# Optimization experiments

Hardware: AMD Instinct MI355X
Metric: run time of the kernel (lower is better)

Reference implementation:

```python
import jax, jax.numpy as jnp
import numpy as np

B, V, D = 8, 2048, 3
CL1_F, CL1_K = 64, 6
CL2_F, CL2_K = 128, 5
F1, F2 = 512, 256


def _uniform(k, shape, fin, fout):
    s = np.sqrt(2.0 / (fin + fout)).astype(np.float32)
    return jax.random.uniform(k, shape, jnp.float32, -s, s)


def setup_inputs() -> dict:
    key = jax.random.key(0)
    ks = jax.random.split(key, 8)
    x = jax.random.normal(ks[0], (B, D, V), jnp.float32)
    # dense stand-in for the scaled graph Laplacian; scaled so spectral radius < 1
    L = jax.random.normal(ks[1], (B, V, V), jnp.float32) * (0.5 / np.sqrt(V))
    L = 0.5 * (L + L.transpose(0, 2, 1))  # symmetric like a real Laplacian
    return {
        "x": x,
        "L": L,
        "cl1_w": _uniform(ks[2], (CL1_F, D * CL1_K), CL1_K, CL1_F),
        "cl1_b": jnp.zeros((CL1_F,), jnp.float32),
        "cl2_w": _uniform(ks[3], (CL2_F, CL2_K * CL1_F), CL2_K * CL1_F, CL2_F),
        "cl2_b": jnp.zeros((CL2_F,), jnp.float32),
        "fc1_w": _uniform(ks[4], (F1, CL2_F), CL2_F, F1),
        "fc1_b": jnp.zeros((F1,), jnp.float32),
        "fc2_w": _uniform(ks[5], (F2, F1), F1, F2),
        "fc2_b": jnp.zeros((F2,), jnp.float32),
    }


def _cheby_conv(x, L, W, b, K):
    # x: [B, V, Fin], L: [B, V, V] -> [B, V, Fout]
    x0 = x
    xs = [x0]
    if K > 1:
        x1 = jnp.einsum('bvu,buf->bvf', L, x0)
        xs.append(x1)
    for _ in range(2, K):
        x2 = 2.0 * jnp.einsum('bvu,buf->bvf', L, x1) - x0
        xs.append(x2)
        x0, x1 = x1, x2
    # torch ordering: feature index = fin * K + k  -> stack K on last axis
    xk = jnp.stack(xs, axis=-1)                 # [B, V, Fin, K]
    xk = xk.reshape(xk.shape[0], xk.shape[1], -1)  # [B, V, Fin*K]
    return xk @ W.T + b


def reference(x, L, cl1_w, cl1_b, cl2_w, cl2_b, fc1_w, fc1_b, fc2_w, fc2_b):
    xp = x.transpose(0, 2, 1)                    # [B, V, D]
    y = jax.nn.relu(_cheby_conv(xp, L, cl1_w, cl1_b, CL1_K))
    y = jax.nn.relu(_cheby_conv(y, L, cl2_w, cl2_b, CL2_K))
    y = jax.nn.relu(y @ fc1_w.T + fc1_b)
    y = jax.nn.relu(y @ fc2_w.T + fc2_b)
    return y                                     # [B, V, F2]
```

## Files before the change

### kernel.cpp

```cpp
#include <hip/hip_runtime.h>

#define B_ 8
#define V_ 2048
#define D_ 3
#define M_ (B_*V_)

typedef __attribute__((ext_vector_type(8))) short short8;
typedef __attribute__((ext_vector_type(4))) float f32x4;

__device__ inline void async_copy16(const void* g, void* lds) {
  __builtin_amdgcn_global_load_lds(
      (const __attribute__((address_space(1))) unsigned int*)g,
      (__attribute__((address_space(3))) unsigned int*)lds, 16, 0, 0);
}

__device__ inline void split_bf16(float v, short& hi, short& lo) {
  unsigned u  = __float_as_uint(v);
  unsigned hb = u & 0xFFFF0000u;
  float d = v - __uint_as_float(hb);
  hi = (short)(hb >> 16);
  lo = (short)(__float_as_uint(d) >> 16);
}

__global__ __launch_bounds__(256) void k_prep(
    const float* __restrict__ x,
    const float* __restrict__ w1, const float* __restrict__ w2,
    const float* __restrict__ fw1, const float* __restrict__ fw2,
    float* __restrict__ xa,
    short* __restrict__ XKh, short* __restrict__ XKl,
    short* __restrict__ w1h, short* __restrict__ w1l,
    short* __restrict__ w2h, short* __restrict__ w2l,
    short* __restrict__ fw1h, short* __restrict__ fw1l,
    short* __restrict__ fw2h, short* __restrict__ fw2l) {
  int i = blockIdx.x * 256 + threadIdx.x;
  short hi, lo;
  if (i < M_*64) {
    int r = i >> 6, s = i & 63;
    float val = 0.f;
    if (s == 0 || s == 6 || s == 12) {
      int f = s / 6;
      int b = r >> 11, v = r & (V_-1);
      val = x[((size_t)b*D_ + f)*V_ + v];
      xa[(size_t)r*3 + f] = val;
    }
    split_bf16(val, hi, lo);
    XKh[i] = hi; XKl[i] = lo;
    return;
  }
  i -= M_*64;
  if (i < 4096) {
    int n = i >> 6, k = i & 63;
    float v = (k < 18) ? w1[n*18 + k] : 0.f;
    split_bf16(v, hi, lo); w1h[i] = hi; w1l[i] = lo; return;
  }
  i -= 4096;
  if (i < 40960) { split_bf16(w2[i],  hi, lo); w2h[i]=hi;  w2l[i]=lo;  return; }
  i -= 40960;
  if (i < 65536) { split_bf16(fw1[i], hi, lo); fw1h[i]=hi; fw1l[i]=lo; return; }
  i -= 65536;
  if (i < 131072){ split_bf16(fw2[i], hi, lo); fw2h[i]=hi; fw2l[i]=lo; return; }
}

__global__ __launch_bounds__(256) void k_cheby1(const float* __restrict__ L,
    const float* __restrict__ xc, const float* __restrict__ xp,
    float* __restrict__ xn, short* __restrict__ XKh, short* __restrict__ XKl,
    float alpha, float beta, int kidx) {
  __shared__ float sx[3][V_];
  int b  = blockIdx.x >> 7;
  int r0 = (blockIdx.x & 127) * 16;
  const float* xcb = xc + (size_t)b*V_*D_;
  for (int i = threadIdx.x; i < V_*D_; i += 256) {
    int u = i / 3, f = i - u*3;
    sx[f][u] = xcb[i];
  }
  __syncthreads();
  int w = threadIdx.x >> 6, lane = threadIdx.x & 63;
  const float4* X0 = (const float4*)sx[0];
  const float4* X1 = (const float4*)sx[1];
  const float4* X2 = (const float4*)sx[2];
  int rbase = r0 + w*4;
  const float4* Lr[4];
  #pragma unroll
  for (int rr = 0; rr < 4; rr++)
    Lr[rr] = (const float4*)(L + ((size_t)b*V_ + rbase + rr)*V_);

  float acc[4][3] = {{0.f,0.f,0.f},{0.f,0.f,0.f},{0.f,0.f,0.f},{0.f,0.f,0.f}};

  #pragma unroll 2
  for (int it = 0; it < 8; it++) {
    int u4 = it*64 + lane;
    float4 x0 = X0[u4], x1 = X1[u4], x2 = X2[u4];
    #pragma unroll
    for (int rr = 0; rr < 4; rr++) {
      float4 lv = Lr[rr][u4];
      acc[rr][0] = fmaf(lv.x,x0.x,fmaf(lv.y,x0.y,fmaf(lv.z,x0.z,fmaf(lv.w,x0.w,acc[rr][0]))));
      acc[rr][1] = fmaf(lv.x,x1.x,fmaf(lv.y,x1.y,fmaf(lv.z,x1.z,fmaf(lv.w,x1.w,acc[rr][1]))));
      acc[rr][2] = fmaf(lv.x,x2.x,fmaf(lv.y,x2.y,fmaf(lv.z,x2.z,fmaf(lv.w,x2.w,acc[rr][2]))));
    }
  }
  #pragma unroll
  for (int off = 32; off > 0; off >>= 1)
    #pragma unroll
    for (int rr = 0; rr < 4; rr++)
      #pragma unroll
      for (int f = 0; f < 3; f++)
        acc[rr][f] += __shfl_down(acc[rr][f], off);

  if (lane == 0) {
    size_t base = ((size_t)b*V_ + rbase)*3;
    float v[12];
    #pragma unroll
    for (int rr = 0; rr < 4; rr++)
      #pragma unroll
      for (int f = 0; f < 3; f++)
        v[rr*3+f] = alpha*acc[rr][f];
    if (beta != 0.f) {
      const float4* xp4 = (const float4*)(xp + base);
      float4 p0 = xp4[0], p1 = xp4[1], p2 = xp4[2];
      v[0] -= beta*p0.x; v[1]  -= beta*p0.y; v[2]  -= beta*p0.z; v[3]  -= beta*p0.w;
      v[4] -= beta*p1.x; v[5]  -= beta*p1.y; v[6]  -= beta*p1.z; v[7]  -= beta*p1.w;
      v[8] -= beta*p2.x; v[9]  -= beta*p2.y; v[10] -= beta*p2.z; v[11] -= beta*p2.w;
    }
    float4* xn4 = (float4*)(xn + base);
    xn4[0] = make_float4(v[0], v[1], v[2],  v[3]);
    xn4[1] = make_float4(v[4], v[5], v[6],  v[7]);
    xn4[2] = make_float4(v[8], v[9], v[10], v[11]);
    #pragma unroll
    for (int rr = 0; rr < 4; rr++)
      #pragma unroll
      for (int f = 0; f < 3; f++) {
        short hi, lo; split_bf16(v[rr*3+f], hi, lo);
        size_t o = ((size_t)b*V_ + rbase + rr)*64 + f*6 + kidx;
        XKh[o] = hi; XKl[o] = lo;
      }
  }
}

__global__ __launch_bounds__(256) void k_cheby2_mfma(const float* __restrict__ L,
    const short* __restrict__ Zth, const short* __restrict__ Ztl,
    const float* __restrict__ Zp,
    float* __restrict__ Zn, short* __restrict__ ZKh, short* __restrict__ ZKl,
    short* __restrict__ Znth, short* __restrict__ Zntl,
    float alpha, float beta, int kidx) {
  __shared__ float sA[2][16*64];
  __shared__ short sBh[2][64*64];
  __shared__ short sBl[2][64*64];

  int b  = blockIdx.x >> 7;
  int r0 = (blockIdx.x & 127) * 16;
  const float* Lb   = L   + (size_t)b*V_*V_;
  const short* Zthb = Zth + (size_t)b*64*V_;
  const short* Ztlb = Ztl + (size_t)b*64*V_;

  int tid  = threadIdx.x;
  int w    = tid >> 6;
  int lane = tid & 63;
  int lm   = lane & 15;
  int quad = lane >> 4;
  int cbase = w * 16;

  int rS  = tid >> 4;
  int cS  = (tid & 15) ^ rS;
  size_t gA  = (size_t)(r0 + rS)*V_ + cS*4;
  int nS0 = tid >> 3;
  int cS0 = (tid & 7) ^ (nS0 & 7);
  size_t gB0 = (size_t)nS0*V_ + cS0*8;
  int fS1 = 256 + tid;
  int nS1 = fS1 >> 3;
  int cS1 = (fS1 & 7) ^ (nS1 & 7);
  size_t gB1 = (size_t)nS1*V_ + cS1*8;

  auto stage = [&](int bb, int k0) {
    async_copy16(Lb   + gA  + k0, &sA[bb][tid*4]);
    async_copy16(Zthb + gB0 + k0, &sBh[bb][tid*8]);
    async_copy16(Ztlb + gB0 + k0, &sBl[bb][tid*8]);
    async_copy16(Zthb + gB1 + k0, &sBh[bb][fS1*8]);
    async_copy16(Ztlb + gB1 + k0, &sBl[bb][fS1*8]);
  };

  f32x4 acc = {0.f,0.f,0.f,0.f};

  stage(0, 0);
  __syncthreads();

  for (int s = 0; s < V_/64; s++) {
    int bb = s & 1;
    if (s < V_/64 - 1) stage(bb ^ 1, (s+1)*64);

    const f32x4*  sAv  = (const f32x4*)sA[bb];
    const short8* sBhv = (const short8*)sBh[bb];
    const short8* sBlv = (const short8*)sBl[bb];

    #pragma unroll
    for (int ks = 0; ks < 2; ks++) {
      int koff = ks * 32;
      int r = lm;
      int ca = (koff >> 2) + 2*quad;
      f32x4 a0 = sAv[r*16 + (ca ^ r)];
      f32x4 a1 = sAv[r*16 + ((ca + 1) ^ r)];
      float av[8] = {a0.x, a0.y, a0.z, a0.w, a1.x, a1.y, a1.z, a1.w};
      short8 ah, al;
      #pragma unroll
      for (int j = 0; j < 8; j++) {
        short hi, lo; split_bf16(av[j], hi, lo);
        ah[j] = hi; al[j] = lo;
      }
      int cb = (koff >> 3) + quad;
      int n = cbase + lm;
      short8 bh = sBhv[n*8 + (cb ^ (n & 7))];
      short8 bl = sBlv[n*8 + (cb ^ (n & 7))];
      acc = __builtin_amdgcn_mfma_f32_16x16x32_bf16(ah, bh, acc, 0, 0, 0);
      acc = __builtin_amdgcn_mfma_f32_16x16x32_bf16(ah, bl, acc, 0, 0, 0);
      acc = __builtin_amdgcn_mfma_f32_16x16x32_bf16(al, bh, acc, 0, 0, 0);
    }
    __syncthreads();
  }

  int n = cbase + lm;
  #pragma unroll
  for (int i = 0; i < 4; i++) {
    int r = r0 + quad*4 + i;
    size_t rowb = (size_t)b*V_ + r;
    float v = alpha * acc[i];
    if (beta != 0.f) v -= beta * Zp[rowb*64 + n];
    Zn[rowb*64 + n] = v;
    short hi, lo; split_bf16(v, hi, lo);
    size_t ok = rowb*320 + (size_t)n*5 + kidx;
    ZKh[ok] = hi; ZKl[ok] = lo;
    size_t o = ((size_t)b*64 + n)*V_ + r;
    Znth[o] = hi; Zntl[o] = lo;
  }
}

__device__ __forceinline__ void gemm_tile(
    const short* __restrict__ Ah, const short* __restrict__ Al,
    const short* __restrict__ Wh, const short* __restrict__ Wl,
    const float* __restrict__ bias, int N, int K, int row0, int col0,
    short* sAh, short* sAl, short* sWh, short* sWl,
    float* __restrict__ Cf, short* __restrict__ Ch, short* __restrict__ Cl,
    short* __restrict__ Ph, short* __restrict__ Pl, int packMul, int packStride,
    short* __restrict__ Th, short* __restrict__ Tl) {
  int tid = threadIdx.x, w = tid >> 6, lane = tid & 63;
  int lm = lane & 15, quad = lane >> 4;
  int wm = (w & 1) * 32, wn = (w >> 1) * 32;

  const short8* vAh = (const short8*)sAh;
  const short8* vAl = (const short8*)sAl;
  const short8* vWh = (const short8*)sWh;
  const short8* vWl = (const short8*)sWl;

  f32x4 acc[2][2] = {{{0.f,0.f,0.f,0.f},{0.f,0.f,0.f,0.f}},
                     {{0.f,0.f,0.f,0.f},{0.f,0.f,0.f,0.f}}};

  for (int k0 = 0; k0 < K; k0 += 64) {
    if (k0) __syncthreads();
    #pragma unroll
    for (int t = 0; t < 2; t++) {
      int f = t*256 + tid;
      int r = f >> 3, p = f & 7;
      int c = p ^ (r & 7);
      size_t goA = (size_t)(row0 + r)*K + k0 + c*8;
      size_t goW = (size_t)(col0 + r)*K + k0 + c*8;
      async_copy16(Ah + goA, &sAh[f*8]);
      async_copy16(Al + goA, &sAl[f*8]);
      async_copy16(Wh + goW, &sWh[f*8]);
      async_copy16(Wl + goW, &sWl[f*8]);
    }
    __syncthreads();

    #pragma unroll
    for (int ks = 0; ks < 2; ks++) {
      int kc = ks*4 + quad;
      short8 a_h[2], a_l[2], b_h[2], b_l[2];
      #pragma unroll
      for (int i = 0; i < 2; i++) {
        int m = wm + i*16 + lm;
        a_h[i] = vAh[m*8 + (kc ^ (m & 7))];
        a_l[i] = vAl[m*8 + (kc ^ (m & 7))];
      }
      #pragma unroll
      for (int j = 0; j < 2; j++) {
        int n = wn + j*16 + lm;
        b_h[j] = vWh[n*8 + (kc ^ (n & 7))];
        b_l[j] = vWl[n*8 + (kc ^ (n & 7))];
      }
      #pragma unroll
      for (int i = 0; i < 2; i++)
        #pragma unroll
        for (int j = 0; j < 2; j++) {
          acc[i][j] = __builtin_amdgcn_mfma_f32_16x16x32_bf16(a_h[i], b_h[j], acc[i][j], 0, 0, 0);
          acc[i][j] = __builtin_amdgcn_mfma_f32_16x16x32_bf16(a_h[i], b_l[j], acc[i][j], 0, 0, 0);
          acc[i][j] = __builtin_amdgcn_mfma_f32_16x16x32_bf16(a_l[i], b_h[j], acc[i][j], 0, 0, 0);
        }
    }
  }

  #pragma unroll
  for (int i = 0; i < 2; i++)
    #pragma unroll
    for (int j = 0; j < 2; j++) {
      int col = col0 + wn + j*16 + lm;
      float bj = bias[col];
      #pragma unroll
      for (int g = 0; g < 4; g++) {
        int row = row0 + wm + i*16 + quad*4 + g;
        float v = acc[i][j][g] + bj;
        v = v > 0.f ? v : 0.f;
        if (Cf) Cf[(size_t)row*N + col] = v;
        short hi, lo;
        if (Ch || Ph || Th) split_bf16(v, hi, lo);
        if (Ch) {
          Ch[(size_t)row*N + col] = hi;
          Cl[(size_t)row*N + col] = lo;
        }
        if (Ph) {
          size_t o = (size_t)row*packStride + (size_t)col*packMul;
          Ph[o] = hi; Pl[o] = lo;
        }
        if (Th) {
          int bb = row >> 11, vv = row & (V_-1);
          size_t o = ((size_t)bb*64 + col)*V_ + vv;
          Th[o] = hi; Tl[o] = lo;
        }
      }
    }
}

__global__ __launch_bounds__(256) void k_gemm_y1(
    const short* __restrict__ XKh, const short* __restrict__ XKl,
    const short* __restrict__ w1h, const short* __restrict__ w1l,
    const float* __restrict__ b1, float* __restrict__ y1,
    short* __restrict__ ZKh, short* __restrict__ ZKl,
    short* __restrict__ Th, short* __restrict__ Tl) {
  __shared__ short sAh[64*64], sAl[64*64], sWh[64*64], sWl[64*64];
  gemm_tile(XKh, XKl, w1h, w1l, b1, 64, 64, blockIdx.x*64, 0,
            sAh, sAl, sWh, sWl,
            y1, nullptr, nullptr, ZKh, ZKl, 5, 320, Th, Tl);
}

__global__ __launch_bounds__(256) void k_gemm_bf16(
    const short* __restrict__ Ah, const short* __restrict__ Al,
    const short* __restrict__ Wh, const short* __restrict__ Wl,
    const float* __restrict__ bias, int N, int K,
    float* __restrict__ Cf, short* __restrict__ Ch, short* __restrict__ Cl) {
  __shared__ short sAh[64*64], sAl[64*64], sWh[64*64], sWl[64*64];
  int bm = blockIdx.x & 255;
  int bn = blockIdx.x >> 8;
  gemm_tile(Ah, Al, Wh, Wl, bias, N, K, bm*64, bn*64,
            sAh, sAl, sWh, sWl,
            Cf, Ch, Cl, nullptr, nullptr, 0, 0, nullptr, nullptr);
}

extern "C" void kernel_launch(void* const* d_in, const int* in_sizes, int n_in,
                              void* d_out, int out_size, void* d_ws, size_t ws_size,
                              hipStream_t stream) {
  const float* x   = (const float*)d_in[0];
  const float* L   = (const float*)d_in[1];
  const float* w1  = (const float*)d_in[2];
  const float* b1  = (const float*)d_in[3];
  const float* w2  = (const float*)d_in[4];
  const float* b2  = (const float*)d_in[5];
  const float* fw1 = (const float*)d_in[6];
  const float* fb1 = (const float*)d_in[7];
  const float* fw2 = (const float*)d_in[8];
  const float* fb2 = (const float*)d_in[9];
  float* out = (float*)d_out;

  float* p  = (float*)d_ws;
  float* xa = p;  p += (size_t)B_*V_*D_;
  float* xb = p;  p += (size_t)B_*V_*D_;
  float* xc = p;  p += (size_t)B_*V_*D_;
  float* y1 = p;  p += (size_t)M_*64;
  float* zb = p;  p += (size_t)M_*64;
  float* zc = p;  p += (size_t)M_*64;
  short* sp = (short*)p;
  short* ZKh = sp;  sp += (size_t)M_*320;
  short* ZKl = sp;  sp += (size_t)M_*320;
  short* y2h = sp;  sp += (size_t)M_*128;
  short* y2l = sp;  sp += (size_t)M_*128;
  short* h1h = sp;  sp += (size_t)M_*512;
  short* h1l = sp;  sp += (size_t)M_*512;
  short* ZtAh = sp; sp += (size_t)M_*64;
  short* ZtAl = sp; sp += (size_t)M_*64;
  short* ZtBh = sp; sp += (size_t)M_*64;
  short* ZtBl = sp; sp += (size_t)M_*64;
  short* w1h = sp;  sp += 64*64;
  short* w1l = sp;  sp += 64*64;
  short* w2h = sp;  sp += 128*320;
  short* w2l = sp;  sp += 128*320;
  short* fw1h = sp; sp += 512*128;
  short* fw1l = sp; sp += 512*128;
  short* fw2h = sp; sp += 256*512;
  short* fw2l = sp; sp += 256*512;
  short* XKh = h1h;
  short* XKl = h1h + (size_t)M_*64;

  k_prep<<<5040, 256, 0, stream>>>(x, w1, w2, fw1, fw2, xa,
                                   XKh, XKl, w1h, w1l, w2h, w2l,
                                   fw1h, fw1l, fw2h, fw2l);

  k_cheby1<<<1024, 256, 0, stream>>>(L, xa, xa, xb, XKh, XKl, 1.f, 0.f, 1);
  k_cheby1<<<1024, 256, 0, stream>>>(L, xb, xa, xc, XKh, XKl, 2.f, 1.f, 2);
  k_cheby1<<<1024, 256, 0, stream>>>(L, xc, xb, xa, XKh, XKl, 2.f, 1.f, 3);
  k_cheby1<<<1024, 256, 0, stream>>>(L, xa, xc, xb, XKh, XKl, 2.f, 1.f, 4);
  k_cheby1<<<1024, 256, 0, stream>>>(L, xb, xa, xc, XKh, XKl, 2.f, 1.f, 5);

  k_gemm_y1<<<256, 256, 0, stream>>>(XKh, XKl, w1h, w1l, b1,
                                     y1, ZKh, ZKl, ZtAh, ZtAl);

  k_cheby2_mfma<<<1024, 256, 0, stream>>>(L, ZtAh, ZtAl, y1, zb, ZKh, ZKl,
                                          ZtBh, ZtBl, 1.f, 0.f, 1);
  k_cheby2_mfma<<<1024, 256, 0, stream>>>(L, ZtBh, ZtBl, y1, zc, ZKh, ZKl,
                                          ZtAh, ZtAl, 2.f, 1.f, 2);
  k_cheby2_mfma<<<1024, 256, 0, stream>>>(L, ZtAh, ZtAl, zb, y1, ZKh, ZKl,
                                          ZtBh, ZtBl, 2.f, 1.f, 3);
  k_cheby2_mfma<<<1024, 256, 0, stream>>>(L, ZtBh, ZtBl, zc, zb, ZKh, ZKl,
                                          ZtAh, ZtAl, 2.f, 1.f, 4);

  k_gemm_bf16<<<512, 256, 0, stream>>>(ZKh, ZKl, w2h, w2l, b2, 128, 320,
                                       nullptr, y2h, y2l);
  k_gemm_bf16<<<2048, 256, 0, stream>>>(y2h, y2l, fw1h, fw1l, fb1, 512, 128,
                                        nullptr, h1h, h1l);
  k_gemm_bf16<<<1024, 256, 0, stream>>>(h1h, h1l, fw2h, fw2l, fb2, 256, 512,
                                        out, nullptr, nullptr);
}
```

Measured before the change: 536.6 us.

## Double row tile in cheby2 MFMA kernel and interleave batch across blocks

Each cheby2 block now computes 32 rows instead of 16, so every staged Z tile in LDS is reused by two MFMA row-tiles. This halves the grid and the total re-reads of the transposed Z operand. The main loop now uses a single waitcnt plus barrier per step instead of two __syncthreads, and raises wave priority around the MFMA group. Block indexing in cheby1 and cheby2 now interleaves the batch index across consecutive blocks to spread L reads across batches. The risks are lower occupancy from the larger LDS footprint and fewer blocks, and more register use from the doubled accumulators.

Result: no change. 536.4 us (-0.0%).

```diff
diff --git a/kernel.cpp b/kernel.cpp
--- a/kernel.cpp
+++ b/kernel.cpp
@@ -66,8 +66,8 @@
     float* __restrict__ xn, short* __restrict__ XKh, short* __restrict__ XKl,
     float alpha, float beta, int kidx) {
   __shared__ float sx[3][V_];
-  int b  = blockIdx.x >> 7;
-  int r0 = (blockIdx.x & 127) * 16;
+  int b  = blockIdx.x & 7;
+  int r0 = (blockIdx.x >> 3) * 16;
   const float* xcb = xc + (size_t)b*V_*D_;
   for (int i = threadIdx.x; i < V_*D_; i += 256) {
     int u = i / 3, f = i - u*3;
@@ -142,12 +142,12 @@
     float* __restrict__ Zn, short* __restrict__ ZKh, short* __restrict__ ZKl,
     short* __restrict__ Znth, short* __restrict__ Zntl,
     float alpha, float beta, int kidx) {
-  __shared__ float sA[2][16*64];
+  __shared__ float sA[2][32*64];
   __shared__ short sBh[2][64*64];
   __shared__ short sBl[2][64*64];
 
-  int b  = blockIdx.x >> 7;
-  int r0 = (blockIdx.x & 127) * 16;
+  int b  = blockIdx.x & 7;
+  int r0 = (blockIdx.x >> 3) * 32;
   const float* Lb   = L   + (size_t)b*V_*V_;
   const short* Zthb = Zth + (size_t)b*64*V_;
   const short* Ztlb = Ztl + (size_t)b*64*V_;
@@ -159,32 +159,34 @@
   int quad = lane >> 4;
   int cbase = w * 16;
 
-  int rS  = tid >> 4;
-  int cS  = (tid & 15) ^ rS;
-  size_t gA  = (size_t)(r0 + rS)*V_ + cS*4;
-  int nS0 = tid >> 3;
-  int cS0 = (tid & 7) ^ (nS0 & 7);
-  size_t gB0 = (size_t)nS0*V_ + cS0*8;
-  int fS1 = 256 + tid;
-  int nS1 = fS1 >> 3;
-  int cS1 = (fS1 & 7) ^ (nS1 & 7);
-  size_t gB1 = (size_t)nS1*V_ + cS1*8;
+  int f1  = tid + 256;
+  int rA0 = tid >> 4, cA0 = (tid & 15) ^ (rA0 & 15);
+  int rA1 = f1 >> 4,  cA1 = (f1 & 15) ^ (rA1 & 15);
+  size_t gA0 = (size_t)(r0 + rA0)*V_ + cA0*4;
+  size_t gA1 = (size_t)(r0 + rA1)*V_ + cA1*4;
+  int nB0 = tid >> 3, cB0 = (tid & 7) ^ (nB0 & 7);
+  int nB1 = f1 >> 3,  cB1 = (f1 & 7) ^ (nB1 & 7);
+  size_t gB0 = (size_t)nB0*V_ + cB0*8;
+  size_t gB1 = (size_t)nB1*V_ + cB1*8;
 
   auto stage = [&](int bb, int k0) {
-    async_copy16(Lb   + gA  + k0, &sA[bb][tid*4]);
+    async_copy16(Lb   + gA0 + k0, &sA[bb][tid*4]);
+    async_copy16(Lb   + gA1 + k0, &sA[bb][f1*4]);
     async_copy16(Zthb + gB0 + k0, &sBh[bb][tid*8]);
     async_copy16(Ztlb + gB0 + k0, &sBl[bb][tid*8]);
-    async_copy16(Zthb + gB1 + k0, &sBh[bb][fS1*8]);
-    async_copy16(Ztlb + gB1 + k0, &sBl[bb][fS1*8]);
+    async_copy16(Zthb + gB1 + k0, &sBh[bb][f1*8]);
+    async_copy16(Ztlb + gB1 + k0, &sBl[bb][f1*8]);
   };
 
-  f32x4 acc = {0.f,0.f,0.f,0.f};
+  f32x4 acc[2] = {{0.f,0.f,0.f,0.f},{0.f,0.f,0.f,0.f}};
 
   stage(0, 0);
-  __syncthreads();
 
   for (int s = 0; s < V_/64; s++) {
     int bb = s & 1;
+    asm volatile("s_waitcnt vmcnt(0)" ::: "memory");
+    __builtin_amdgcn_s_barrier();
+    __builtin_amdgcn_sched_barrier(0);
     if (s < V_/64 - 1) stage(bb ^ 1, (s+1)*64);
 
     const f32x4*  sAv  = (const f32x4*)sA[bb];
@@ -194,41 +196,51 @@
     #pragma unroll
     for (int ks = 0; ks < 2; ks++) {
       int koff = ks * 32;
-      int r = lm;
-      int ca = (koff >> 2) + 2*quad;
-      f32x4 a0 = sAv[r*16 + (ca ^ r)];
-      f32x4 a1 = sAv[r*16 + ((ca + 1) ^ r)];
-      float av[8] = {a0.x, a0.y, a0.z, a0.w, a1.x, a1.y, a1.z, a1.w};
-      short8 ah, al;
-      #pragma unroll
-      for (int j = 0; j < 8; j++) {
-        short hi, lo; split_bf16(av[j], hi, lo);
-        ah[j] = hi; al[j] = lo;
+      short8 ah[2], al[2];
+      #pragma unroll
+      for (int t = 0; t < 2; t++) {
+        int r = t*16 + lm;
+        int ca = (koff >> 2) + 2*quad;
+        f32x4 a0 = sAv[r*16 + (ca ^ (r & 15))];
+        f32x4 a1 = sAv[r*16 + ((ca + 1) ^ (r & 15))];
+        float av[8] = {a0.x, a0.y, a0.z, a0.w, a1.x, a1.y, a1.z, a1.w};
+        #pragma unroll
+        for (int j = 0; j < 8; j++) {
+          short hi, lo; split_bf16(av[j], hi, lo);
+          ah[t][j] = hi; al[t][j] = lo;
+        }
       }
       int cb = (koff >> 3) + quad;
       int n = cbase + lm;
       short8 bh = sBhv[n*8 + (cb ^ (n & 7))];
       short8 bl = sBlv[n*8 + (cb ^ (n & 7))];
-      acc = __builtin_amdgcn_mfma_f32_16x16x32_bf16(ah, bh, acc, 0, 0, 0);
-      acc = __builtin_amdgcn_mfma_f32_16x16x32_bf16(ah, bl, acc, 0, 0, 0);
-      acc = __builtin_amdgcn_mfma_f32_16x16x32_bf16(al, bh, acc, 0, 0, 0);
-    }
-    __syncthreads();
+      __builtin_amdgcn_s_setprio(1);
+      #pragma unroll
+      for (int t = 0; t < 2; t++) {
+        acc[t] = __builtin_amdgcn_mfma_f32_16x16x32_bf16(ah[t], bh, acc[t], 0, 0, 0);
+        acc[t] = __builtin_amdgcn_mfma_f32_16x16x32_bf16(ah[t], bl, acc[t], 0, 0, 0);
+        acc[t] = __builtin_amdgcn_mfma_f32_16x16x32_bf16(al[t], bh, acc[t], 0, 0, 0);
+      }
+      __builtin_amdgcn_s_setprio(0);
+    }
   }
 
   int n = cbase + lm;
   #pragma unroll
-  for (int i = 0; i < 4; i++) {
-    int r = r0 + quad*4 + i;
-    size_t rowb = (size_t)b*V_ + r;
-    float v = alpha * acc[i];
-    if (beta != 0.f) v -= beta * Zp[rowb*64 + n];
-    Zn[rowb*64 + n] = v;
-    short hi, lo; split_bf16(v, hi, lo);
-    size_t ok = rowb*320 + (size_t)n*5 + kidx;
-    ZKh[ok] = hi; ZKl[ok] = lo;
-    size_t o = ((size_t)b*64 + n)*V_ + r;
-    Znth[o] = hi; Zntl[o] = lo;
+  for (int t = 0; t < 2; t++) {
+    #pragma unroll
+    for (int i = 0; i < 4; i++) {
+      int r = r0 + t*16 + quad*4 + i;
+      size_t rowb = (size_t)b*V_ + r;
+      float v = alpha * acc[t][i];
+      if (beta != 0.f) v -= beta * Zp[rowb*64 + n];
+      Zn[rowb*64 + n] = v;
+      short hi, lo; split_bf16(v, hi, lo);
+      size_t ok = rowb*320 + (size_t)n*5 + kidx;
+      ZKh[ok] = hi; ZKl[ok] = lo;
+      size_t o = ((size_t)b*64 + n)*V_ + r;
+      Znth[o] = hi; Zntl[o] = lo;
+    }
   }
 }
 
@@ -408,14 +420,14 @@
   k_gemm_y1<<<256, 256, 0, stream>>>(XKh, XKl, w1h, w1l, b1,
                                      y1, ZKh, ZKl, ZtAh, ZtAl);
 
-  k_cheby2_mfma<<<1024, 256, 0, stream>>>(L, ZtAh, ZtAl, y1, zb, ZKh, ZKl,
-                                          ZtBh, ZtBl, 1.f, 0.f, 1);
-  k_cheby2_mfma<<<1024, 256, 0, stream>>>(L, ZtBh, ZtBl, y1, zc, ZKh, ZKl,
-                                          ZtAh, ZtAl, 2.f, 1.f, 2);
-  k_cheby2_mfma<<<1024, 256, 0, stream>>>(L, ZtAh, ZtAl, zb, y1, ZKh, ZKl,
-                                          ZtBh, ZtBl, 2.f, 1.f, 3);
-  k_cheby2_mfma<<<1024, 256, 0, stream>>>(L, ZtBh, ZtBl, zc, zb, ZKh, ZKl,
-                                          ZtAh, ZtAl, 2.f, 1.f, 4);
+  k_cheby2_mfma<<<512, 256, 0, stream>>>(L, ZtAh, ZtAl, y1, zb, ZKh, ZKl,
+                                         ZtBh, ZtBl, 1.f, 0.f, 1);
+  k_cheby2_mfma<<<512, 256, 0, stream>>>(L, ZtBh, ZtBl, y1, zc, ZKh, ZKl,
+                                         ZtAh, ZtAl, 2.f, 1.f, 2);
+  k_cheby2_mfma<<<512, 256, 0, stream>>>(L, ZtAh, ZtAl, zb, y1, ZKh, ZKl,
+                                         ZtBh, ZtBl, 2.f, 1.f, 3);
+  k_cheby2_mfma<<<512, 256, 0, stream>>>(L, ZtBh, ZtBl, zc, zb, ZKh, ZKl,
+                                         ZtAh, ZtAl, 2.f, 1.f, 4);
 
   k_gemm_bf16<<<512, 256, 0, stream>>>(ZKh, ZKl, w2h, w2l, b2, 128, 320,
                                        nullptr, y2h, y2l);
```
